# Performance work log

Hardware: AMD Instinct MI355X
Metric: run time of the kernel (lower is better)

Reference implementation:

```python
import jax, jax.numpy as jnp
import numpy as np

B, C, H, W = 8, 64, 256, 256


def setup_inputs() -> dict:
    key = jax.random.key(0)
    ks = jax.random.split(key, 7)
    return {
        "x": jax.random.normal(ks[0], (B, C, H, W), dtype=jnp.float32),
        "query_w": jax.random.normal(ks[1], (C, W, W), dtype=jnp.float32),
        "key_w": jax.random.normal(ks[2], (C, W, W), dtype=jnp.float32),
        "var_w": jax.random.normal(ks[3], (C, W, W), dtype=jnp.float32),
        "query_b": jax.random.normal(ks[4], (C, H, W), dtype=jnp.float32),
        "key_b": jax.random.normal(ks[5], (C, H, W), dtype=jnp.float32),
        "var_b": jax.random.normal(ks[6], (C, H, W), dtype=jnp.float32),
    }


def reference(x, query_w, key_w, var_w, query_b, key_b, var_b):
    # mode == 'horizontal': per-channel right-matmul over the W axis.
    # x: [B,C,H,W], *_w: [C,W,W] (broadcast over batch), *_b: [C,H,W].
    q = jnp.einsum("bchw,cwv->bchv", x, query_w) + query_b
    k = jnp.einsum("bchw,cwv->bchv", x, key_w) + key_b
    v = jnp.einsum("bchw,cwv->bchv", x, var_w) + var_b
    return jax.nn.softmax(q * k, axis=-1) * v
```

## Files before the change

kernel.cpp:

```cpp
#include <hip/hip_runtime.h>
#include <math.h>


#define Bn 8
#define Cn 64
#define Hn 256
#define Wn 256

typedef _Float16 f16x8 __attribute__((ext_vector_type(8)));
typedef _Float16 f16x4 __attribute__((ext_vector_type(4)));
typedef float    f32x16 __attribute__((ext_vector_type(16)));

#define MFMA(a, b, c) __builtin_amdgcn_mfma_f32_32x32x16_f16((a), (b), (c), 0, 0, 0)

#define WS_PLANE_H 4096
#define WS_NEED ((size_t)Cn * 16 * 5 * 8192)

#define FTILE 40960

__device__ __forceinline__ void ldst16(const void* g, void* l) {
    __builtin_amdgcn_global_load_lds(
        (const __attribute__((address_space(1))) unsigned int*)g,
        (__attribute__((address_space(3))) unsigned int*)l, 16, 0, 0);
}

__device__ __forceinline__ void cvt_hilo(const float4 a, const float4 b,
                                         f16x8& hi, f16x8& lo) {
    float v[8] = {a.x, a.y, a.z, a.w, b.x, b.y, b.z, b.w};
#pragma unroll
    for (int e = 0; e < 8; ++e) {
        _Float16 hv = (_Float16)v[e];
        hi[e] = hv;
        lo[e] = (_Float16)(v[e] - (float)hv);
    }
}

__global__ __launch_bounds__(256) void prep_w(
    const float* __restrict__ wq, const float* __restrict__ wk,
    const float* __restrict__ wv, _Float16* __restrict__ wf)
{
    const int blk = blockIdx.x;
    const int kt  = blk & 15;
    const int c   = blk >> 4;
    const int n   = threadIdx.x;
    const int ntile = n >> 5;
    const int nl    = n & 31;

    _Float16* base = wf + (size_t)blk * 5 * WS_PLANE_H;
    const size_t woff = ((size_t)c * Wn + kt * 16) * Wn + n;

#pragma unroll
    for (int mat = 0; mat < 2; ++mat) {
        const float* Wp = (mat ? wk : wq) + woff;
        float w16[16];
#pragma unroll
        for (int r = 0; r < 16; ++r)
            w16[r] = Wp[(size_t)r * Wn];
        _Float16* hip = base + (mat * 2) * WS_PLANE_H + ntile * 512;
        _Float16* lop = hip + WS_PLANE_H;
#pragma unroll
        for (int h2 = 0; h2 < 2; ++h2) {
            f16x8 hi8, lo8;
#pragma unroll
            for (int e = 0; e < 8; ++e) {
                const float wv_ = w16[h2 * 8 + e];
                _Float16 hv = (_Float16)wv_;
                hi8[e] = hv;
                lo8[e] = (_Float16)(wv_ - (float)hv);
            }
            *(f16x8*)(hip + (h2 * 32 + nl) * 8) = hi8;
            *(f16x8*)(lop + (h2 * 32 + nl) * 8) = lo8;
        }
    }
    {
        const float* Wp = wv + woff;
        float w16[16];
#pragma unroll
        for (int r = 0; r < 16; ++r)
            w16[r] = Wp[(size_t)r * Wn];
        _Float16* vp = base + 4 * WS_PLANE_H + ntile * 512;
#pragma unroll
        for (int h2 = 0; h2 < 2; ++h2) {
            f16x8 hi8;
#pragma unroll
            for (int e = 0; e < 8; ++e)
                hi8[e] = (_Float16)w16[h2 * 8 + e];
            *(f16x8*)(vp + (h2 * 32 + nl) * 8) = hi8;
        }
    }
}

__global__ __launch_bounds__(1024, 4) void axile_attn_pipe(
    const float* __restrict__ x,
    const _Float16* __restrict__ wf,
    const float* __restrict__ bq,
    const float* __restrict__ bk,
    const float* __restrict__ bv,
    float* __restrict__ out)
{
    __shared__ __align__(16) char lds[3 * FTILE];

    const int tid   = threadIdx.x;
    const int lane  = tid & 63;
    const int h     = lane >> 5;
    const int l31   = lane & 31;
    const int wv_id = tid >> 6;
    const int ncol  = wv_id & 7;
    const int mt    = wv_id >> 3;

    const int blk = blockIdx.x;
    const int c   = blk & 63;
    const int j   = blk >> 6;
    const int b   = j & 7;
    const int h0  = (j >> 3) * 64;

    const float* xrow = x + ((size_t)(b * Cn + c) * Hn + h0 + mt * 32 + l31) * Wn + h * 8;
    const char*  wfc  = (const char*)(wf + (size_t)c * 16 * 5 * WS_PLANE_H);

    const bool halfw = (tid < 512);
    const int  so0 = tid * 16;
    const int  so1 = 16384 + tid * 16;
    const int  so2 = 32768 + tid * 16;

    f32x16 accq, acck, accv;
#pragma unroll
    for (int r = 0; r < 16; ++r) {
        accq[r] = 0.f;
        acck[r] = 0.f;
        accv[r] = 0.f;
    }

    f16x8 ah, al;
    {
        const float4 xa = *(const float4*)(xrow);
        const float4 xb = *(const float4*)(xrow + 4);
        ldst16(wfc + so0, lds + so0);
        ldst16(wfc + so1, lds + so1);
        if (halfw) ldst16(wfc + so2, lds + so2);
        const char* s1 = wfc + FTILE;
        ldst16(s1 + so0, lds + FTILE + so0);
        ldst16(s1 + so1, lds + FTILE + so1);
        if (halfw) ldst16(s1 + so2, lds + FTILE + so2);
        cvt_hilo(xa, xb, ah, al);
    }
    if (halfw) asm volatile("s_waitcnt vmcnt(3)" ::: "memory");
    else       asm volatile("s_waitcnt vmcnt(2)" ::: "memory");
    __builtin_amdgcn_s_barrier();
    __builtin_amdgcn_sched_barrier(0);

    int o_cur = 0, o_nxt = FTILE, o_sta = 2 * FTILE;
    for (int kt = 0; kt < 16; ++kt) {
        float4 ya, yb;
        if (kt < 15) {
            ya = *(const float4*)(xrow + (kt + 1) * 16);
            yb = *(const float4*)(xrow + (kt + 1) * 16 + 4);
        }
        if (kt < 14) {
            const char* ssrc = wfc + (size_t)(kt + 2) * FTILE;
            ldst16(ssrc + so0, lds + o_sta + so0);
            ldst16(ssrc + so1, lds + o_sta + so1);
            if (halfw) ldst16(ssrc + so2, lds + o_sta + so2);
        }

        const char* bb = lds + o_cur + ncol * 1024 + lane * 16;
        const f16x8 bqh = *(const f16x8*)(bb);
        const f16x8 bql = *(const f16x8*)(bb + 8192);
        const f16x8 bkh = *(const f16x8*)(bb + 16384);
        const f16x8 bkl = *(const f16x8*)(bb + 24576);
        const f16x8 bvh = *(const f16x8*)(bb + 32768);

        accq = MFMA(ah, bqh, accq);
        accq = MFMA(al, bqh, accq);
        accq = MFMA(ah, bql, accq);
        acck = MFMA(ah, bkh, acck);
        acck = MFMA(al, bkh, acck);
        acck = MFMA(ah, bkl, acck);
        accv = MFMA(ah, bvh, accv);

        if (kt < 15)
            cvt_hilo(ya, yb, ah, al);

        if (kt < 14) {
            if (halfw) asm volatile("s_waitcnt vmcnt(3)" ::: "memory");
            else       asm volatile("s_waitcnt vmcnt(2)" ::: "memory");
        } else if (kt == 14) {
            asm volatile("s_waitcnt vmcnt(0)" ::: "memory");
        }
        __builtin_amdgcn_s_barrier();
        __builtin_amdgcn_sched_barrier(0);
        const int t = o_cur; o_cur = o_nxt; o_nxt = o_sta; o_sta = t;
    }

    float* part    = (float*)lds;
    float* combmax = (float*)(lds + 2048);
    float* combsum = (float*)(lds + 2304);

#pragma unroll
    for (int r = 0; r < 16; ++r) {
        const int row = mt * 32 + (r & 3) + 8 * (r >> 2) + 4 * h;
        const int vv  = ncol * 32 + l31;
        const size_t bidx = ((size_t)c * Hn + h0 + row) * Wn + vv;
        const float qv = accq[r] + bq[bidx];
        const float kv = acck[r] + bk[bidx];
        accq[r] = qv * kv;
    }

#pragma unroll
    for (int r = 0; r < 16; ++r) {
        float m2 = accq[r];
#pragma unroll
        for (int off = 16; off > 0; off >>= 1)
            m2 = fmaxf(m2, __shfl_xor(m2, off, 64));
        if ((lane & 31) == r) {
            const int row = mt * 32 + (r & 3) + 8 * (r >> 2) + 4 * h;
            part[ncol * 64 + row] = m2;
        }
    }
    __syncthreads();
    if (tid < 64) {
        float m = part[tid];
#pragma unroll
        for (int w = 1; w < 8; ++w)
            m = fmaxf(m, part[w * 64 + tid]);
        combmax[tid] = m;
    }
    __syncthreads();

#pragma unroll
    for (int r = 0; r < 16; ++r) {
        const int row = mt * 32 + (r & 3) + 8 * (r >> 2) + 4 * h;
        const float mx = combmax[row];
        const float e0 = __expf(accq[r] - mx);
        accq[r] = e0;
        float ps = e0;
#pragma unroll
        for (int off = 16; off > 0; off >>= 1)
            ps += __shfl_xor(ps, off, 64);
        if ((lane & 31) == r)
            part[ncol * 64 + row] = ps;
    }
    __syncthreads();
    if (tid < 64) {
        float s = part[tid];
#pragma unroll
        for (int w = 1; w < 8; ++w)
            s += part[w * 64 + tid];
        combsum[tid] = s;
    }
    __syncthreads();

    float* obase = out + ((size_t)(b * Cn + c) * Hn) * Wn;
#pragma unroll
    for (int r = 0; r < 16; ++r) {
        const int row = mt * 32 + (r & 3) + 8 * (r >> 2) + 4 * h;
        const float inv = 1.0f / combsum[row];
        const int hh = h0 + row;
        const int vv = ncol * 32 + l31;
        const size_t bidx = ((size_t)c * Hn + hh) * Wn + vv;
        const float vx = accv[r] + bv[bidx];
        obase[(size_t)hh * Wn + vv] = accq[r] * vx * inv;
    }
}

#define LDS_ALO 2048
#define LDS_B   4096

__global__ __launch_bounds__(512, 4) void axile_attn_mfma4(
    const float* __restrict__ x,
    const float* __restrict__ wq,
    const float* __restrict__ wk,
    const float* __restrict__ wv,
    const float* __restrict__ bq,
    const float* __restrict__ bk,
    const float* __restrict__ bv,
    float* __restrict__ out)
{
    __shared__ __align__(16) char lds[39424];

    const int tid  = threadIdx.x;
    const int ncol = tid >> 6;
    const int lane = tid & 63;
    const int h    = lane >> 5;
    const int l31  = lane & 31;

    const int blk = blockIdx.x;
    const int c   = blk & 63;
    const int j   = blk >> 6;
    const int b   = j & 7;
    const int h0  = (j >> 3) * 64;

    const float* xbase = x + ((size_t)(b * Cn + c) * Hn + h0) * Wn;
    const float* w_q = wq + (size_t)c * Wn * Wn;
    const float* w_k = wk + (size_t)c * Wn * Wn;
    const float* w_v = wv + (size_t)c * Wn * Wn;

    const int wkh = tid >> 8;
    const int n   = tid & 255;
    const int ntW = n >> 5;
    const int nl  = n & 31;
    const int wfo = ((wkh << 5) | nl) * 16;
    const int am    = tid >> 2;
    const int akq   = tid & 3;
    const int amt   = am >> 5;
    const int alc   = ((akq >> 1) << 5) | (am & 31);
    const int aboff = (akq & 1) * 8;

    f32x16 accq[2], acck[2];
#pragma unroll
    for (int mtx = 0; mtx < 2; ++mtx)
#pragma unroll
        for (int r = 0; r < 16; ++r) {
            accq[mtx][r] = 0.f;
            acck[mtx][r] = 0.f;
        }

    for (int kt = 0; kt < 16; ++kt) {
        const int k0 = kt * 16;
        __syncthreads();
#pragma unroll
        for (int mat = 0; mat < 2; ++mat) {
            const float* Wp = mat ? w_k : w_q;
            const float* wrow = Wp + (size_t)(k0 + wkh * 8) * Wn + n;
            float w8[8];
#pragma unroll
            for (int r = 0; r < 8; ++r)
                w8[r] = wrow[(size_t)r * Wn];
            f16x8 hi8, lo8;
#pragma unroll
            for (int e = 0; e < 8; ++e) {
                const float wv_ = w8[e];
                _Float16 hv = (_Float16)wv_;
                hi8[e] = hv;
                lo8[e] = (_Float16)(wv_ - (float)hv);
            }
            char* dplane = lds + LDS_B + (mat * 2) * 8192 + ntW * 1024;
            *(f16x8*)(dplane + wfo) = hi8;
            *(f16x8*)(dplane + 8192 + wfo) = lo8;
        }
        if (tid < 256) {
            const float4 xx = *(const float4*)(xbase + (size_t)am * Wn + k0 + akq * 4);
            f16x4 hi4, lo4;
            _Float16 t0 = (_Float16)xx.x; hi4[0] = t0; lo4[0] = (_Float16)(xx.x - (float)t0);
            _Float16 t1 = (_Float16)xx.y; hi4[1] = t1; lo4[1] = (_Float16)(xx.y - (float)t1);
            _Float16 t2 = (_Float16)xx.z; hi4[2] = t2; lo4[2] = (_Float16)(xx.z - (float)t2);
            _Float16 t3 = (_Float16)xx.w; hi4[3] = t3; lo4[3] = (_Float16)(xx.w - (float)t3);
            *(f16x4*)(lds + amt * 1024 + alc * 16 + aboff) = hi4;
            *(f16x4*)(lds + LDS_ALO + amt * 1024 + alc * 16 + aboff) = lo4;
        }
        __syncthreads();

        f16x8 ah[2], al[2];
#pragma unroll
        for (int mtx = 0; mtx < 2; ++mtx) {
            ah[mtx] = *(const f16x8*)(lds + mtx * 1024 + lane * 16);
            al[mtx] = *(const f16x8*)(lds + LDS_ALO + mtx * 1024 + lane * 16);
        }
        const char* bb = lds + LDS_B + ncol * 1024 + lane * 16;
        f16x8 bqh = *(const f16x8*)(bb + 0 * 8192);
        f16x8 bql = *(const f16x8*)(bb + 1 * 8192);
        f16x8 bkh = *(const f16x8*)(bb + 2 * 8192);
        f16x8 bkl = *(const f16x8*)(bb + 3 * 8192);
#pragma unroll
        for (int mtx = 0; mtx < 2; ++mtx) {
            accq[mtx] = MFMA(ah[mtx], bqh, accq[mtx]);
            accq[mtx] = MFMA(al[mtx], bqh, accq[mtx]);
            accq[mtx] = MFMA(ah[mtx], bql, accq[mtx]);
            acck[mtx] = MFMA(ah[mtx], bkh, acck[mtx]);
            acck[mtx] = MFMA(al[mtx], bkh, acck[mtx]);
            acck[mtx] = MFMA(ah[mtx], bkl, acck[mtx]);
        }
    }

    float* part    = (float*)(lds + 36864);
    float* combmax = (float*)(lds + 36864 + 2048);
    float* combsum = (float*)(lds + 36864 + 2304);

#pragma unroll
    for (int mtx = 0; mtx < 2; ++mtx)
#pragma unroll
        for (int r = 0; r < 16; ++r) {
            const int rl = (r & 3) + 8 * (r >> 2) + 4 * h;
            const int hh = h0 + mtx * 32 + rl;
            const int vv = ncol * 32 + l31;
            const size_t bidx = ((size_t)c * Hn + hh) * Wn + vv;
            const float qv = accq[mtx][r] + bq[bidx];
            const float kv = acck[mtx][r] + bk[bidx];
            accq[mtx][r] = qv * kv;
        }

#pragma unroll
    for (int mtx = 0; mtx < 2; ++mtx)
#pragma unroll
        for (int r = 0; r < 16; ++r) {
            float m2 = accq[mtx][r];
#pragma unroll
            for (int off = 16; off > 0; off >>= 1)
                m2 = fmaxf(m2, __shfl_xor(m2, off, 64));
            if ((lane & 15) == r && ((lane >> 4) & 1) == mtx) {
                const int rl  = (r & 3) + 8 * (r >> 2) + 4 * h;
                const int row = mtx * 32 + rl;
                part[ncol * 64 + row] = m2;
            }
        }
    __syncthreads();
    if (tid < 64) {
        float m = part[tid];
#pragma unroll
        for (int w = 1; w < 8; ++w)
            m = fmaxf(m, part[w * 64 + tid]);
        combmax[tid] = m;
    }
    __syncthreads();

#pragma unroll
    for (int mtx = 0; mtx < 2; ++mtx)
#pragma unroll
        for (int r = 0; r < 16; ++r) {
            const int rl  = (r & 3) + 8 * (r >> 2) + 4 * h;
            const int row = mtx * 32 + rl;
            const float mx = combmax[row];
            const float e0 = __expf(accq[mtx][r] - mx);
            accq[mtx][r] = e0;
            float ps = e0;
#pragma unroll
            for (int off = 16; off > 0; off >>= 1)
                ps += __shfl_xor(ps, off, 64);
            if ((lane & 15) == r && ((lane >> 4) & 1) == mtx)
                part[ncol * 64 + row] = ps;
        }
    __syncthreads();
    if (tid < 64) {
        float s = part[tid];
#pragma unroll
        for (int w = 1; w < 8; ++w)
            s += part[w * 64 + tid];
        combsum[tid] = s;
    }

    f32x16 accv[2];
#pragma unroll
    for (int mtx = 0; mtx < 2; ++mtx)
#pragma unroll
        for (int r = 0; r < 16; ++r)
            accv[mtx][r] = 0.f;

    for (int kt = 0; kt < 16; ++kt) {
        const int k0 = kt * 16;
        __syncthreads();
        {
            const float* wrow = w_v + (size_t)(k0 + wkh * 8) * Wn + n;
            float w8[8];
#pragma unroll
            for (int r = 0; r < 8; ++r)
                w8[r] = wrow[(size_t)r * Wn];
            f16x8 hi8;
#pragma unroll
            for (int e = 0; e < 8; ++e)
                hi8[e] = (_Float16)w8[e];
            *(f16x8*)(lds + LDS_B + ntW * 1024 + wfo) = hi8;
        }
        if (tid < 256) {
            const float4 xx = *(const float4*)(xbase + (size_t)am * Wn + k0 + akq * 4);
            f16x4 hi4;
            hi4[0] = (_Float16)xx.x;
            hi4[1] = (_Float16)xx.y;
            hi4[2] = (_Float16)xx.z;
            hi4[3] = (_Float16)xx.w;
            *(f16x4*)(lds + amt * 1024 + alc * 16 + aboff) = hi4;
        }
        __syncthreads();

        f16x8 ah[2];
#pragma unroll
        for (int mtx = 0; mtx < 2; ++mtx)
            ah[mtx] = *(const f16x8*)(lds + mtx * 1024 + lane * 16);
        f16x8 bvh = *(const f16x8*)(lds + LDS_B + ncol * 1024 + lane * 16);
#pragma unroll
        for (int mtx = 0; mtx < 2; ++mtx)
            accv[mtx] = MFMA(ah[mtx], bvh, accv[mtx]);
    }

    float* obase = out + ((size_t)(b * Cn + c) * Hn) * Wn;
#pragma unroll
    for (int mtx = 0; mtx < 2; ++mtx)
#pragma unroll
        for (int r = 0; r < 16; ++r) {
            const int rl  = (r & 3) + 8 * (r >> 2) + 4 * h;
            const int row = mtx * 32 + rl;
            const float inv = 1.0f / combsum[row];
            const int hh = h0 + row;
            const int vv = ncol * 32 + l31;
            const size_t bidx = ((size_t)c * Hn + hh) * Wn + vv;
            const float vx = accv[mtx][r] + bv[bidx];
            obase[(size_t)hh * Wn + vv] = accq[mtx][r] * vx * inv;
        }
}

extern "C" void kernel_launch(void* const* d_in, const int* in_sizes, int n_in,
                              void* d_out, int out_size, void* d_ws, size_t ws_size,
                              hipStream_t stream) {
    (void)in_sizes; (void)n_in; (void)out_size;
    const float* x  = (const float*)d_in[0];
    const float* wq = (const float*)d_in[1];
    const float* wk = (const float*)d_in[2];
    const float* wv = (const float*)d_in[3];
    const float* bq = (const float*)d_in[4];
    const float* bk = (const float*)d_in[5];
    const float* bv = (const float*)d_in[6];
    float* out = (float*)d_out;

    if (d_ws != nullptr && ws_size >= WS_NEED) {
        hipLaunchKernelGGL(prep_w, dim3(Cn * 16), dim3(256), 0, stream,
                           wq, wk, wv, (_Float16*)d_ws);
        hipLaunchKernelGGL(axile_attn_pipe, dim3(Bn * 4 * Cn), dim3(1024), 0, stream,
                           x, (const _Float16*)d_ws, bq, bk, bv, out);
    } else {
        hipLaunchKernelGGL(axile_attn_mfma4, dim3(Bn * 4 * Cn), dim3(512), 0, stream,
                           x, wq, wk, wv, bq, bk, bv, out);
    }
}
```

Baseline: 559.3 us.

## Stage whole x tile in LDS as fp16 hi/lo and double-buffer weights

New measurement: 481.3 us. -13.9%, faster.

```diff
diff --git a/kernel.cpp b/kernel.cpp
--- a/kernel.cpp
+++ b/kernel.cpp
@@ -15,8 +15,11 @@
 
 #define WS_PLANE_H 4096
 #define WS_NEED ((size_t)Cn * 16 * 5 * 8192)
-
 #define FTILE 40960
+
+#define XSTRIDE 2064
+#define XLO_OFF 33024
+#define WB0     66048
 
 __device__ __forceinline__ void ldst16(const void* g, void* l) {
     __builtin_amdgcn_global_load_lds(
@@ -24,11 +27,10 @@
         (__attribute__((address_space(3))) unsigned int*)l, 16, 0, 0);
 }
 
-__device__ __forceinline__ void cvt_hilo(const float4 a, const float4 b,
-                                         f16x8& hi, f16x8& lo) {
-    float v[8] = {a.x, a.y, a.z, a.w, b.x, b.y, b.z, b.w};
-#pragma unroll
-    for (int e = 0; e < 8; ++e) {
+__device__ __forceinline__ void cvt_hilo4(const float4 a, f16x4& hi, f16x4& lo) {
+    float v[4] = {a.x, a.y, a.z, a.w};
+#pragma unroll
+    for (int e = 0; e < 4; ++e) {
         _Float16 hv = (_Float16)v[e];
         hi[e] = hv;
         lo[e] = (_Float16)(v[e] - (float)hv);
@@ -90,7 +92,7 @@
     }
 }
 
-__global__ __launch_bounds__(1024, 4) void axile_attn_pipe(
+__global__ __launch_bounds__(1024, 1) void axile_attn_xlds(
     const float* __restrict__ x,
     const _Float16* __restrict__ wf,
     const float* __restrict__ bq,
@@ -98,7 +100,7 @@
     const float* __restrict__ bv,
     float* __restrict__ out)
 {
-    __shared__ __align__(16) char lds[3 * FTILE];
+    __shared__ __align__(16) char lds[147968];
 
     const int tid   = threadIdx.x;
     const int lane  = tid & 63;
@@ -114,8 +116,7 @@
     const int b   = j & 7;
     const int h0  = (j >> 3) * 64;
 
-    const float* xrow = x + ((size_t)(b * Cn + c) * Hn + h0 + mt * 32 + l31) * Wn + h * 8;
-    const char*  wfc  = (const char*)(wf + (size_t)c * 16 * 5 * WS_PLANE_H);
+    const char* wfc = (const char*)(wf + (size_t)c * 16 * 5 * WS_PLANE_H);
 
     const bool halfw = (tid < 512);
     const int  so0 = tid * 16;
@@ -130,38 +131,48 @@
         accv[r] = 0.f;
     }
 
-    f16x8 ah, al;
     {
-        const float4 xa = *(const float4*)(xrow);
-        const float4 xb = *(const float4*)(xrow + 4);
-        ldst16(wfc + so0, lds + so0);
-        ldst16(wfc + so1, lds + so1);
-        if (halfw) ldst16(wfc + so2, lds + so2);
-        const char* s1 = wfc + FTILE;
-        ldst16(s1 + so0, lds + FTILE + so0);
-        ldst16(s1 + so1, lds + FTILE + so1);
-        if (halfw) ldst16(s1 + so2, lds + FTILE + so2);
-        cvt_hilo(xa, xb, ah, al);
-    }
-    if (halfw) asm volatile("s_waitcnt vmcnt(3)" ::: "memory");
-    else       asm volatile("s_waitcnt vmcnt(2)" ::: "memory");
-    __builtin_amdgcn_s_barrier();
-    __builtin_amdgcn_sched_barrier(0);
-
-    int o_cur = 0, o_nxt = FTILE, o_sta = 2 * FTILE;
+        const char* xg = (const char*)(x + ((size_t)(b * Cn + c) * Hn + h0) * Wn);
+        float4 xv0 = *(const float4*)(xg + (size_t)tid * 16);
+        float4 xv1 = *(const float4*)(xg + (size_t)(tid + 1024) * 16);
+        float4 xv2 = *(const float4*)(xg + (size_t)(tid + 2048) * 16);
+        float4 xv3 = *(const float4*)(xg + (size_t)(tid + 3072) * 16);
+        ldst16(wfc + so0, lds + WB0 + so0);
+        ldst16(wfc + so1, lds + WB0 + so1);
+        if (halfw) ldst16(wfc + so2, lds + WB0 + so2);
+
+        const int k0  = (tid & 63) * 4;
+        const int xkt = k0 >> 4;
+        const int hp  = (k0 >> 3) & 1;
+        const int bo  = (k0 & 7) * 2;
+        const int xbase = xkt * XSTRIDE + bo;
+        float4 xv[4] = {xv0, xv1, xv2, xv3};
+#pragma unroll
+        for (int i = 0; i < 4; ++i) {
+            const int r    = (tid >> 6) + i * 16;
+            const int slot = (r >> 5) * 64 + hp * 32 + (r & 31);
+            f16x4 h4, l4;
+            cvt_hilo4(xv[i], h4, l4);
+            *(f16x4*)(lds + xbase + slot * 16) = h4;
+            *(f16x4*)(lds + XLO_OFF + xbase + slot * 16) = l4;
+        }
+        asm volatile("s_waitcnt vmcnt(0)" ::: "memory");
+        __builtin_amdgcn_s_barrier();
+        __builtin_amdgcn_sched_barrier(0);
+    }
+
+    const int aslot = (mt * 64 + h * 32 + l31) * 16;
+    int o_cur = WB0, o_nxt = WB0 + FTILE;
     for (int kt = 0; kt < 16; ++kt) {
-        float4 ya, yb;
         if (kt < 15) {
-            ya = *(const float4*)(xrow + (kt + 1) * 16);
-            yb = *(const float4*)(xrow + (kt + 1) * 16 + 4);
-        }
-        if (kt < 14) {
-            const char* ssrc = wfc + (size_t)(kt + 2) * FTILE;
-            ldst16(ssrc + so0, lds + o_sta + so0);
-            ldst16(ssrc + so1, lds + o_sta + so1);
-            if (halfw) ldst16(ssrc + so2, lds + o_sta + so2);
-        }
-
+            const char* ssrc = wfc + (size_t)(kt + 1) * FTILE;
+            ldst16(ssrc + so0, lds + o_nxt + so0);
+            ldst16(ssrc + so1, lds + o_nxt + so1);
+            if (halfw) ldst16(ssrc + so2, lds + o_nxt + so2);
+        }
+
+        const f16x8 ah = *(const f16x8*)(lds + kt * XSTRIDE + aslot);
+        const f16x8 al = *(const f16x8*)(lds + XLO_OFF + kt * XSTRIDE + aslot);
         const char* bb = lds + o_cur + ncol * 1024 + lane * 16;
         const f16x8 bqh = *(const f16x8*)(bb);
         const f16x8 bql = *(const f16x8*)(bb + 8192);
@@ -177,18 +188,10 @@
         acck = MFMA(ah, bkl, acck);
         accv = MFMA(ah, bvh, accv);
 
-        if (kt < 15)
-            cvt_hilo(ya, yb, ah, al);
-
-        if (kt < 14) {
-            if (halfw) asm volatile("s_waitcnt vmcnt(3)" ::: "memory");
-            else       asm volatile("s_waitcnt vmcnt(2)" ::: "memory");
-        } else if (kt == 14) {
-            asm volatile("s_waitcnt vmcnt(0)" ::: "memory");
-        }
+        asm volatile("s_waitcnt vmcnt(0)" ::: "memory");
         __builtin_amdgcn_s_barrier();
         __builtin_amdgcn_sched_barrier(0);
-        const int t = o_cur; o_cur = o_nxt; o_nxt = o_sta; o_sta = t;
+        const int t = o_cur; o_cur = o_nxt; o_nxt = t;
     }
 
     float* part    = (float*)lds;
@@ -512,7 +515,7 @@
     if (d_ws != nullptr && ws_size >= WS_NEED) {
         hipLaunchKernelGGL(prep_w, dim3(Cn * 16), dim3(256), 0, stream,
                            wq, wk, wv, (_Float16*)d_ws);
-        hipLaunchKernelGGL(axile_attn_pipe, dim3(Bn * 4 * Cn), dim3(1024), 0, stream,
+        hipLaunchKernelGGL(axile_attn_xlds, dim3(Bn * 4 * Cn), dim3(1024), 0, stream,
                            x, (const _Float16*)d_ws, bq, bk, bv, out);
     } else {
         hipLaunchKernelGGL(axile_attn_mfma4, dim3(Bn * 4 * Cn), dim3(512), 0, stream,
```
